# Performance work log

Measured on AMD Instinct MI355X. Metric: run time of the kernel, lower is better.

The kernel has to match this reference:

```python
import jax, jax.numpy as jnp
import numpy as np

B, F, V, E, T, NTOK, G, D = 8192, 64, 1000, 64, 2, 16, 4, 256
LN_EPS = 1e-5


def setup_inputs() -> dict:
    key = jax.random.key(0)
    ks = jax.random.split(key, 5)
    int_feats = jax.random.randint(ks[0], (B, F), 0, V, dtype=jnp.int64)
    missing_mask = jax.random.randint(ks[1], (B, F), 0, 2, dtype=jnp.int32)
    # deterministic seeded permutation of features split into NTOK equal groups
    perm = np.random.default_rng(1234).permutation(F)
    group_idx = jnp.asarray(perm.reshape(NTOK, G), dtype=jnp.int32)
    emb_tables = jax.random.normal(ks[2], (T, F, V, E), jnp.float32) * 0.02
    missing_emb = jax.random.normal(ks[3], (T, F, E), jnp.float32) * 0.02
    kW, kb = jax.random.split(ks[4])
    W = jax.random.normal(kW, (D, E * T), jnp.float32) * (1.0 / np.sqrt(E * T))
    b = jnp.zeros((D,), jnp.float32)
    ln_gamma = jnp.ones((D,), jnp.float32)
    ln_beta = jnp.zeros((D,), jnp.float32)
    return {"int_feats": int_feats, "missing_mask": missing_mask,
            "group_idx": group_idx, "emb_tables": emb_tables,
            "missing_emb": missing_emb, "W": W, "b": b,
            "ln_gamma": ln_gamma, "ln_beta": ln_beta}


def reference(int_feats, missing_mask, group_idx, emb_tables, missing_emb, W, b, ln_gamma, ln_beta):
    f_idx = jnp.arange(F)[None, :]  # (1, F) broadcast with (B, F) ids
    # per-table feature embedding gather: [T, B, F, E]
    feats = jax.vmap(lambda tbl: tbl[f_idx, int_feats])(emb_tables)
    # additive missing embeddings
    mask = missing_mask.astype(feats.dtype)
    feats = feats + mask[None, :, :, None] * missing_emb[:, None, :, :]
    # token-group mean pooling: [T, B, NTOK, G, E] -> [T, B, NTOK, E]
    pooled = feats[:, :, group_idx, :].mean(axis=3)
    # concat tables along feature dim (table order preserved): [B, NTOK, T*E]
    x = jnp.moveaxis(pooled, 0, 2).reshape(B, NTOK, T * E)
    # Linear -> SiLU -> LayerNorm
    h = jax.nn.silu(x @ W.T + b)
    mu = h.mean(-1, keepdims=True)
    var = ((h - mu) ** 2).mean(-1, keepdims=True)
    return (h - mu) * jax.lax.rsqrt(var + LN_EPS) * ln_gamma + ln_beta
```

## Files before the change

### kernel.cpp

```cpp
#include <hip/hip_runtime.h>
#include <math.h>

#define B_    8192
#define F_    64
#define V_    1000
#define E_    64
#define T_    2
#define NTOK_ 16
#define G_    4
#define D_    256
#define K_    128
#define LN_EPS 1e-5f

#define R_    4
#define XSP   136

#define EB_ELEMS (T_*F_*V_*E_)
#define MB_ELEMS (T_*F_*E_)
#define WB_ELEMS (D_*K_)

typedef __attribute__((ext_vector_type(8))) short  frag_ab;
typedef __attribute__((ext_vector_type(4))) float  frag_cd;

template<bool BT> struct GVec;
template<> struct GVec<true>  { using T = uint2;  };
template<> struct GVec<false> { using T = float4; };

static __device__ __forceinline__ unsigned short f2bf(float f) {
    unsigned int u = __float_as_uint(f);
    u += 0x7FFFu + ((u >> 16) & 1u);
    return (unsigned short)(u >> 16);
}
static __device__ __forceinline__ unsigned int pk2(float a, float b) {
    return (unsigned int)f2bf(a) | ((unsigned int)f2bf(b) << 16);
}
static __device__ __forceinline__ void g2f(uint2 v, float& a, float& b, float& c, float& d) {
    a = __uint_as_float(v.x << 16);
    b = __uint_as_float(v.x & 0xFFFF0000u);
    c = __uint_as_float(v.y << 16);
    d = __uint_as_float(v.y & 0xFFFF0000u);
}
static __device__ __forceinline__ void g2f(float4 v, float& a, float& b, float& c, float& d) {
    a = v.x; b = v.y; c = v.z; d = v.w;
}

__global__ __launch_bounds__(256) void convert_w_kernel(const float* __restrict__ W,
                                                        unsigned int* __restrict__ Wb_packed) {
    const int i = blockIdx.x * 256 + threadIdx.x;
    if (i < WB_ELEMS / 2) {
        const float2 v = *(const float2*)(W + (size_t)i * 2);
        Wb_packed[i] = pk2(v.x, v.y);
    }
}

__global__ __launch_bounds__(256) void convert_tbl_kernel(const float* __restrict__ emb,
                                                          const float* __restrict__ miss,
                                                          unsigned int* __restrict__ ebp,
                                                          unsigned int* __restrict__ mbp) {
    const int i = blockIdx.x * 256 + threadIdx.x;
    const int neb = EB_ELEMS / 4;
    if (i < neb) {
        const float4 v = *(const float4*)(emb + (size_t)i * 4);
        ebp[2 * i]     = pk2(v.x, v.y);
        ebp[2 * i + 1] = pk2(v.z, v.w);
    } else if (i < neb + MB_ELEMS / 4) {
        const int j = i - neb;
        const float4 v = *(const float4*)(miss + (size_t)j * 4);
        mbp[2 * j]     = pk2(v.x, v.y);
        mbp[2 * j + 1] = pk2(v.z, v.w);
    }
}

template<bool BT, int MINW>
__global__ __launch_bounds__(256, MINW) void fused_tokenizer_kernel(
    const int*   __restrict__ int_feats,
    const int*   __restrict__ missing_mask,
    const int*   __restrict__ group_idx,
    const float* __restrict__ embf,
    const float* __restrict__ missf,
    const unsigned short* __restrict__ embb,
    const unsigned short* __restrict__ missb,
    const unsigned short* __restrict__ Wb,
    const float* __restrict__ bias,
    const float* __restrict__ gamma,
    const float* __restrict__ beta,
    float*       __restrict__ out)
{
    using VT = typename GVec<BT>::T;

    __shared__ unsigned short xs[2][NTOK_][XSP];
    __shared__ unsigned int   soff[R_][F_];
    __shared__ int            sg[F_];
    __shared__ float          part_s [4][NTOK_];
    __shared__ float          part_ss[4][NTOK_];

    const int tid  = threadIdx.x;
    const int lane = tid & 63;
    const int wave = tid >> 6;
    const int mA   = lane & 15;
    const int q    = lane >> 4;
    const int r0   = blockIdx.x * R_;

    {
        const int rr = tid >> 6, f = tid & 63;
        const int id = int_feats[(r0 + rr) * F_ + f];
        const unsigned int mk = (unsigned int)missing_mask[(r0 + rr) * F_ + f];
        soff[rr][f] = (unsigned int)((f * V_ + id) * E_) | (mk << 31);
        if (tid < F_) sg[tid] = group_idx[tid];
    }

    frag_ab wfr[4][4];
    float bias_r[4], gm_r[4], bt_r[4];
#pragma unroll
    for (int t = 0; t < 4; ++t) {
        const int nrow = wave * 64 + t * 16 + mA;
        const unsigned short* wp = Wb + (size_t)nrow * K_ + 8 * q;
#pragma unroll
        for (int s = 0; s < 4; ++s) wfr[t][s] = *(const frag_ab*)(wp + 32 * s);
        bias_r[t] = bias[nrow];
        gm_r[t]   = gamma[nrow];
        bt_r[t]   = beta[nrow];
    }

    __syncthreads();

    VT  mval[2][G_];
    int fidx[2][G_];
#pragma unroll
    for (int i = 0; i < 2; ++i) {
        const int c = i * 256 + tid, n = c >> 5, r4 = c & 31, tt = r4 >> 4, e = (r4 & 15) * 4;
#pragma unroll
        for (int g = 0; g < G_; ++g) {
            const int f = sg[n * G_ + g];
            fidx[i][g] = f;
            const size_t mo = (size_t)(tt * F_ + f) * E_ + e;
            if constexpr (BT) mval[i][g] = *(const uint2*)(missb + mo);
            else              mval[i][g] = *(const float4*)(missf + mo);
        }
    }

    auto gather_issue = [&](int rr, VT (&gbuf)[2][G_]) {
#pragma unroll
        for (int i = 0; i < 2; ++i) {
            const int c = i * 256 + tid, r4 = c & 31, tt = r4 >> 4, e = (r4 & 15) * 4;
            const size_t tb = (size_t)tt * (F_ * V_ * E_) + e;
#pragma unroll
            for (int g = 0; g < G_; ++g) {
                const unsigned int so = soff[rr][fidx[i][g]] & 0x7FFFFFFFu;
                if constexpr (BT) gbuf[i][g] = *(const uint2*)(embb + tb + so);
                else              gbuf[i][g] = *(const float4*)(embf + tb + so);
            }
        }
    };

    auto pack_write = [&](int rr, unsigned short (&dst)[NTOK_][XSP], VT (&gbuf)[2][G_]) {
#pragma unroll
        for (int i = 0; i < 2; ++i) {
            const int c = i * 256 + tid, n = c >> 5, r4 = c & 31;
            float ax = 0.f, ay = 0.f, az = 0.f, aw = 0.f;
#pragma unroll
            for (int g = 0; g < G_; ++g) {
                float vx, vy, vz, vw, mx, my, mz, mw;
                g2f(gbuf[i][g], vx, vy, vz, vw);
                g2f(mval[i][g], mx, my, mz, mw);
                const float mf = (soff[rr][fidx[i][g]] >> 31) ? 1.f : 0.f;
                ax += vx + mf * mx;
                ay += vy + mf * my;
                az += vz + mf * mz;
                aw += vw + mf * mw;
            }
            *(uint2*)(&dst[n][r4 * 4]) =
                make_uint2(pk2(0.25f * ax, 0.25f * ay), pk2(0.25f * az, 0.25f * aw));
        }
    };

    VT g0[2][G_], g1[2][G_];
    gather_issue(0, g0);

#pragma unroll
    for (int r = 0; r < R_; ++r) {
        if (r + 1 < R_) gather_issue(r + 1, g1);

        pack_write(r, xs[r & 1], g0);
        __syncthreads();

        frag_ab a[4];
#pragma unroll
        for (int s = 0; s < 4; ++s)
            a[s] = *(const frag_ab*)(&xs[r & 1][mA][32 * s + 8 * q]);

        float hv[4][4];
        float ps[4]  = {0.f, 0.f, 0.f, 0.f};
        float pss[4] = {0.f, 0.f, 0.f, 0.f};
#pragma unroll
        for (int t = 0; t < 4; ++t) {
            frag_cd acc = {0.f, 0.f, 0.f, 0.f};
#pragma unroll
            for (int s = 0; s < 4; ++s)
                acc = __builtin_amdgcn_mfma_f32_16x16x32_bf16(a[s], wfr[t][s], acc, 0, 0, 0);
#pragma unroll
            for (int reg = 0; reg < 4; ++reg) {
                const float z = acc[reg] + bias_r[t];
                const float h = z / (1.f + __expf(-z));
                hv[t][reg] = h;
                ps[reg]  += h;
                pss[reg] += h * h;
            }
        }

#pragma unroll
        for (int off = 1; off < 16; off <<= 1) {
#pragma unroll
            for (int reg = 0; reg < 4; ++reg) {
                ps[reg]  += __shfl_xor(ps[reg],  off, 64);
                pss[reg] += __shfl_xor(pss[reg], off, 64);
            }
        }
        if (mA == 0) {
            *(float4*)(&part_s [wave][q * 4]) = make_float4(ps[0],  ps[1],  ps[2],  ps[3]);
            *(float4*)(&part_ss[wave][q * 4]) = make_float4(pss[0], pss[1], pss[2], pss[3]);
        }
        __syncthreads();

        const float4 S0 = *(const float4*)(&part_s [0][q * 4]);
        const float4 S1 = *(const float4*)(&part_s [1][q * 4]);
        const float4 S2 = *(const float4*)(&part_s [2][q * 4]);
        const float4 S3 = *(const float4*)(&part_s [3][q * 4]);
        const float4 T0 = *(const float4*)(&part_ss[0][q * 4]);
        const float4 T1 = *(const float4*)(&part_ss[1][q * 4]);
        const float4 T2 = *(const float4*)(&part_ss[2][q * 4]);
        const float4 T3 = *(const float4*)(&part_ss[3][q * 4]);

        float mu[4], rs[4];
        {
            const float s[4]  = {S0.x + S1.x + S2.x + S3.x, S0.y + S1.y + S2.y + S3.y,
                                 S0.z + S1.z + S2.z + S3.z, S0.w + S1.w + S2.w + S3.w};
            const float ss[4] = {T0.x + T1.x + T2.x + T3.x, T0.y + T1.y + T2.y + T3.y,
                                 T0.z + T1.z + T2.z + T3.z, T0.w + T1.w + T2.w + T3.w};
#pragma unroll
            for (int reg = 0; reg < 4; ++reg) {
                mu[reg] = s[reg] * (1.f / D_);
                const float var = ss[reg] * (1.f / D_) - mu[reg] * mu[reg];
                rs[reg] = rsqrtf(var + LN_EPS);
            }
        }

        const size_t obase = (size_t)(r0 + r) * (NTOK_ * D_);
#pragma unroll
        for (int t = 0; t < 4; ++t) {
            const int col = wave * 64 + t * 16 + mA;
            float* op = out + obase + col;
#pragma unroll
            for (int reg = 0; reg < 4; ++reg)
                op[(size_t)(q * 4 + reg) * D_] =
                    (hv[t][reg] - mu[reg]) * rs[reg] * gm_r[t] + bt_r[t];
        }

#pragma unroll
        for (int i = 0; i < 2; ++i)
#pragma unroll
            for (int g = 0; g < G_; ++g) g0[i][g] = g1[i][g];
    }
}

extern "C" void kernel_launch(void* const* d_in, const int* in_sizes, int n_in,
                              void* d_out, int out_size, void* d_ws, size_t ws_size,
                              hipStream_t stream) {
    const int*   int_feats    = (const int*)  d_in[0];
    const int*   missing_mask = (const int*)  d_in[1];
    const int*   group_idx    = (const int*)  d_in[2];
    const float* emb_tables   = (const float*)d_in[3];
    const float* missing_emb  = (const float*)d_in[4];
    const float* W            = (const float*)d_in[5];
    const float* bias         = (const float*)d_in[6];
    const float* gamma        = (const float*)d_in[7];
    const float* beta         = (const float*)d_in[8];
    float* out = (float*)d_out;

    unsigned short* Wb = (unsigned short*)d_ws;
    convert_w_kernel<<<(WB_ELEMS / 2 + 255) / 256, 256, 0, stream>>>(W, (unsigned int*)Wb);

    const size_t need = 2ull * (WB_ELEMS + MB_ELEMS + EB_ELEMS);
    if (ws_size >= need) {
        unsigned short* Mb = Wb + WB_ELEMS;
        unsigned short* Eb = Mb + MB_ELEMS;
        const int nch = (EB_ELEMS + MB_ELEMS) / 4;
        convert_tbl_kernel<<<(nch + 255) / 256, 256, 0, stream>>>(
            emb_tables, missing_emb, (unsigned int*)Eb, (unsigned int*)Mb);
        fused_tokenizer_kernel<true, 3><<<B_ / R_, 256, 0, stream>>>(
            int_feats, missing_mask, group_idx, nullptr, nullptr, Eb, Mb,
            Wb, bias, gamma, beta, out);
    } else {
        fused_tokenizer_kernel<false, 2><<<B_ / R_, 256, 0, stream>>>(
            int_feats, missing_mask, group_idx, emb_tables, missing_emb, nullptr, nullptr,
            Wb, bias, gamma, beta, out);
    }
}
```

Measured before the change: 262.1 us.

## Process one batch row per block instead of four with software-pipelined gathers

After: 245.1 us. -6.5%, faster.

```diff
diff --git a/kernel.cpp b/kernel.cpp
--- a/kernel.cpp
+++ b/kernel.cpp
@@ -12,7 +12,6 @@
 #define K_    128
 #define LN_EPS 1e-5f
 
-#define R_    4
 #define XSP   136
 
 #define EB_ELEMS (T_*F_*V_*E_)
@@ -55,19 +54,17 @@
 
 __global__ __launch_bounds__(256) void convert_tbl_kernel(const float* __restrict__ emb,
                                                           const float* __restrict__ miss,
-                                                          unsigned int* __restrict__ ebp,
-                                                          unsigned int* __restrict__ mbp) {
+                                                          uint2* __restrict__ ebp,
+                                                          uint2* __restrict__ mbp) {
     const int i = blockIdx.x * 256 + threadIdx.x;
     const int neb = EB_ELEMS / 4;
     if (i < neb) {
         const float4 v = *(const float4*)(emb + (size_t)i * 4);
-        ebp[2 * i]     = pk2(v.x, v.y);
-        ebp[2 * i + 1] = pk2(v.z, v.w);
+        ebp[i] = make_uint2(pk2(v.x, v.y), pk2(v.z, v.w));
     } else if (i < neb + MB_ELEMS / 4) {
         const int j = i - neb;
         const float4 v = *(const float4*)(miss + (size_t)j * 4);
-        mbp[2 * j]     = pk2(v.x, v.y);
-        mbp[2 * j + 1] = pk2(v.z, v.w);
+        mbp[j] = make_uint2(pk2(v.x, v.y), pk2(v.z, v.w));
     }
 }
 
@@ -88,178 +85,148 @@
 {
     using VT = typename GVec<BT>::T;
 
-    __shared__ unsigned short xs[2][NTOK_][XSP];
-    __shared__ unsigned int   soff[R_][F_];
+    __shared__ unsigned short xs[NTOK_][XSP];
+    __shared__ unsigned int   soff[F_];
     __shared__ int            sg[F_];
     __shared__ float          part_s [4][NTOK_];
     __shared__ float          part_ss[4][NTOK_];
 
     const int tid  = threadIdx.x;
+    const int b    = blockIdx.x;
     const int lane = tid & 63;
     const int wave = tid >> 6;
     const int mA   = lane & 15;
     const int q    = lane >> 4;
-    const int r0   = blockIdx.x * R_;
-
-    {
-        const int rr = tid >> 6, f = tid & 63;
-        const int id = int_feats[(r0 + rr) * F_ + f];
-        const unsigned int mk = (unsigned int)missing_mask[(r0 + rr) * F_ + f];
-        soff[rr][f] = (unsigned int)((f * V_ + id) * E_) | (mk << 31);
-        if (tid < F_) sg[tid] = group_idx[tid];
-    }
-
-    frag_ab wfr[4][4];
-    float bias_r[4], gm_r[4], bt_r[4];
+
+    if (tid < F_) {
+        const int id = int_feats[b * F_ + tid];
+        const unsigned int mk = (unsigned int)missing_mask[b * F_ + tid];
+        soff[tid] = (unsigned int)((tid * V_ + id) * E_) | (mk << 31);
+        sg[tid]   = group_idx[tid];
+    }
+    __syncthreads();
+
+    VT    gv[2][G_], mv[2][G_];
+    float msk[2][G_];
+#pragma unroll
+    for (int i = 0; i < 2; ++i) {
+        const int c = i * 256 + tid, n = c >> 5, r4 = c & 31, tt = r4 >> 4, e = (r4 & 15) * 4;
+        const unsigned int tb = (unsigned int)(tt * (F_ * V_ * E_)) + e;
+        const unsigned int mb = (unsigned int)(tt * (F_ * E_)) + e;
+#pragma unroll
+        for (int g = 0; g < G_; ++g) {
+            const int f = sg[n * G_ + g];
+            const unsigned int so = soff[f];
+            msk[i][g] = (so >> 31) ? 1.f : 0.f;
+            const unsigned int eo = tb + (so & 0x7FFFFFFFu);
+            const unsigned int mo = mb + (unsigned int)(f * E_);
+            if constexpr (BT) {
+                gv[i][g] = *(const uint2*)(embb + eo);
+                mv[i][g] = *(const uint2*)(missb + mo);
+            } else {
+                gv[i][g] = *(const float4*)(embf + eo);
+                mv[i][g] = *(const float4*)(missf + mo);
+            }
+        }
+    }
+
+#pragma unroll
+    for (int i = 0; i < 2; ++i) {
+        const int c = i * 256 + tid, n = c >> 5, r4 = c & 31;
+        float ax = 0.f, ay = 0.f, az = 0.f, aw = 0.f;
+#pragma unroll
+        for (int g = 0; g < G_; ++g) {
+            float vx, vy, vz, vw, mx, my, mz, mw;
+            g2f(gv[i][g], vx, vy, vz, vw);
+            g2f(mv[i][g], mx, my, mz, mw);
+            const float m = msk[i][g];
+            ax += vx + m * mx;
+            ay += vy + m * my;
+            az += vz + m * mz;
+            aw += vw + m * mw;
+        }
+        *(uint2*)(&xs[n][r4 * 4]) =
+            make_uint2(pk2(0.25f * ax, 0.25f * ay), pk2(0.25f * az, 0.25f * aw));
+    }
+    __syncthreads();
+
+    frag_ab a[4];
+#pragma unroll
+    for (int s = 0; s < 4; ++s)
+        a[s] = *(const frag_ab*)(&xs[mA][32 * s + 8 * q]);
+
+    float hv[4][4];
+    float ps[4]  = {0.f, 0.f, 0.f, 0.f};
+    float pss[4] = {0.f, 0.f, 0.f, 0.f};
+
 #pragma unroll
     for (int t = 0; t < 4; ++t) {
         const int nrow = wave * 64 + t * 16 + mA;
         const unsigned short* wp = Wb + (size_t)nrow * K_ + 8 * q;
-#pragma unroll
-        for (int s = 0; s < 4; ++s) wfr[t][s] = *(const frag_ab*)(wp + 32 * s);
-        bias_r[t] = bias[nrow];
-        gm_r[t]   = gamma[nrow];
-        bt_r[t]   = beta[nrow];
-    }
-
+        frag_cd acc = {0.f, 0.f, 0.f, 0.f};
+#pragma unroll
+        for (int s = 0; s < 4; ++s) {
+            const frag_ab bfr = *(const frag_ab*)(wp + 32 * s);
+            acc = __builtin_amdgcn_mfma_f32_16x16x32_bf16(a[s], bfr, acc, 0, 0, 0);
+        }
+        const float bn = bias[nrow];
+#pragma unroll
+        for (int reg = 0; reg < 4; ++reg) {
+            const float z = acc[reg] + bn;
+            const float h = z / (1.f + __expf(-z));
+            hv[t][reg] = h;
+            ps[reg]  += h;
+            pss[reg] += h * h;
+        }
+    }
+
+#pragma unroll
+    for (int off = 1; off < 16; off <<= 1) {
+#pragma unroll
+        for (int reg = 0; reg < 4; ++reg) {
+            ps[reg]  += __shfl_xor(ps[reg],  off, 64);
+            pss[reg] += __shfl_xor(pss[reg], off, 64);
+        }
+    }
+    if (mA == 0) {
+        *(float4*)(&part_s [wave][q * 4]) = make_float4(ps[0],  ps[1],  ps[2],  ps[3]);
+        *(float4*)(&part_ss[wave][q * 4]) = make_float4(pss[0], pss[1], pss[2], pss[3]);
+    }
     __syncthreads();
 
-    VT  mval[2][G_];
-    int fidx[2][G_];
-#pragma unroll
-    for (int i = 0; i < 2; ++i) {
-        const int c = i * 256 + tid, n = c >> 5, r4 = c & 31, tt = r4 >> 4, e = (r4 & 15) * 4;
-#pragma unroll
-        for (int g = 0; g < G_; ++g) {
-            const int f = sg[n * G_ + g];
-            fidx[i][g] = f;
-            const size_t mo = (size_t)(tt * F_ + f) * E_ + e;
-            if constexpr (BT) mval[i][g] = *(const uint2*)(missb + mo);
-            else              mval[i][g] = *(const float4*)(missf + mo);
-        }
-    }
-
-    auto gather_issue = [&](int rr, VT (&gbuf)[2][G_]) {
-#pragma unroll
-        for (int i = 0; i < 2; ++i) {
-            const int c = i * 256 + tid, r4 = c & 31, tt = r4 >> 4, e = (r4 & 15) * 4;
-            const size_t tb = (size_t)tt * (F_ * V_ * E_) + e;
-#pragma unroll
-            for (int g = 0; g < G_; ++g) {
-                const unsigned int so = soff[rr][fidx[i][g]] & 0x7FFFFFFFu;
-                if constexpr (BT) gbuf[i][g] = *(const uint2*)(embb + tb + so);
-                else              gbuf[i][g] = *(const float4*)(embf + tb + so);
-            }
-        }
-    };
-
-    auto pack_write = [&](int rr, unsigned short (&dst)[NTOK_][XSP], VT (&gbuf)[2][G_]) {
-#pragma unroll
-        for (int i = 0; i < 2; ++i) {
-            const int c = i * 256 + tid, n = c >> 5, r4 = c & 31;
-            float ax = 0.f, ay = 0.f, az = 0.f, aw = 0.f;
-#pragma unroll
-            for (int g = 0; g < G_; ++g) {
-                float vx, vy, vz, vw, mx, my, mz, mw;
-                g2f(gbuf[i][g], vx, vy, vz, vw);
-                g2f(mval[i][g], mx, my, mz, mw);
-                const float mf = (soff[rr][fidx[i][g]] >> 31) ? 1.f : 0.f;
-                ax += vx + mf * mx;
-                ay += vy + mf * my;
-                az += vz + mf * mz;
-                aw += vw + mf * mw;
-            }
-            *(uint2*)(&dst[n][r4 * 4]) =
-                make_uint2(pk2(0.25f * ax, 0.25f * ay), pk2(0.25f * az, 0.25f * aw));
-        }
-    };
-
-    VT g0[2][G_], g1[2][G_];
-    gather_issue(0, g0);
-
-#pragma unroll
-    for (int r = 0; r < R_; ++r) {
-        if (r + 1 < R_) gather_issue(r + 1, g1);
-
-        pack_write(r, xs[r & 1], g0);
-        __syncthreads();
-
-        frag_ab a[4];
-#pragma unroll
-        for (int s = 0; s < 4; ++s)
-            a[s] = *(const frag_ab*)(&xs[r & 1][mA][32 * s + 8 * q]);
-
-        float hv[4][4];
-        float ps[4]  = {0.f, 0.f, 0.f, 0.f};
-        float pss[4] = {0.f, 0.f, 0.f, 0.f};
-#pragma unroll
-        for (int t = 0; t < 4; ++t) {
-            frag_cd acc = {0.f, 0.f, 0.f, 0.f};
-#pragma unroll
-            for (int s = 0; s < 4; ++s)
-                acc = __builtin_amdgcn_mfma_f32_16x16x32_bf16(a[s], wfr[t][s], acc, 0, 0, 0);
-#pragma unroll
-            for (int reg = 0; reg < 4; ++reg) {
-                const float z = acc[reg] + bias_r[t];
-                const float h = z / (1.f + __expf(-z));
-                hv[t][reg] = h;
-                ps[reg]  += h;
-                pss[reg] += h * h;
-            }
-        }
-
-#pragma unroll
-        for (int off = 1; off < 16; off <<= 1) {
-#pragma unroll
-            for (int reg = 0; reg < 4; ++reg) {
-                ps[reg]  += __shfl_xor(ps[reg],  off, 64);
-                pss[reg] += __shfl_xor(pss[reg], off, 64);
-            }
-        }
-        if (mA == 0) {
-            *(float4*)(&part_s [wave][q * 4]) = make_float4(ps[0],  ps[1],  ps[2],  ps[3]);
-            *(float4*)(&part_ss[wave][q * 4]) = make_float4(pss[0], pss[1], pss[2], pss[3]);
-        }
-        __syncthreads();
-
-        const float4 S0 = *(const float4*)(&part_s [0][q * 4]);
-        const float4 S1 = *(const float4*)(&part_s [1][q * 4]);
-        const float4 S2 = *(const float4*)(&part_s [2][q * 4]);
-        const float4 S3 = *(const float4*)(&part_s [3][q * 4]);
-        const float4 T0 = *(const float4*)(&part_ss[0][q * 4]);
-        const float4 T1 = *(const float4*)(&part_ss[1][q * 4]);
-        const float4 T2 = *(const float4*)(&part_ss[2][q * 4]);
-        const float4 T3 = *(const float4*)(&part_ss[3][q * 4]);
-
-        float mu[4], rs[4];
-        {
-            const float s[4]  = {S0.x + S1.x + S2.x + S3.x, S0.y + S1.y + S2.y + S3.y,
-                                 S0.z + S1.z + S2.z + S3.z, S0.w + S1.w + S2.w + S3.w};
-            const float ss[4] = {T0.x + T1.x + T2.x + T3.x, T0.y + T1.y + T2.y + T3.y,
-                                 T0.z + T1.z + T2.z + T3.z, T0.w + T1.w + T2.w + T3.w};
-#pragma unroll
-            for (int reg = 0; reg < 4; ++reg) {
-                mu[reg] = s[reg] * (1.f / D_);
-                const float var = ss[reg] * (1.f / D_) - mu[reg] * mu[reg];
-                rs[reg] = rsqrtf(var + LN_EPS);
-            }
-        }
-
-        const size_t obase = (size_t)(r0 + r) * (NTOK_ * D_);
-#pragma unroll
-        for (int t = 0; t < 4; ++t) {
-            const int col = wave * 64 + t * 16 + mA;
-            float* op = out + obase + col;
-#pragma unroll
-            for (int reg = 0; reg < 4; ++reg)
-                op[(size_t)(q * 4 + reg) * D_] =
-                    (hv[t][reg] - mu[reg]) * rs[reg] * gm_r[t] + bt_r[t];
-        }
-
-#pragma unroll
-        for (int i = 0; i < 2; ++i)
-#pragma unroll
-            for (int g = 0; g < G_; ++g) g0[i][g] = g1[i][g];
+    const float4 S0 = *(const float4*)(&part_s [0][q * 4]);
+    const float4 S1 = *(const float4*)(&part_s [1][q * 4]);
+    const float4 S2 = *(const float4*)(&part_s [2][q * 4]);
+    const float4 S3 = *(const float4*)(&part_s [3][q * 4]);
+    const float4 T0 = *(const float4*)(&part_ss[0][q * 4]);
+    const float4 T1 = *(const float4*)(&part_ss[1][q * 4]);
+    const float4 T2 = *(const float4*)(&part_ss[2][q * 4]);
+    const float4 T3 = *(const float4*)(&part_ss[3][q * 4]);
+
+    float mu[4], rs[4];
+    {
+        const float s[4]  = {S0.x + S1.x + S2.x + S3.x, S0.y + S1.y + S2.y + S3.y,
+                             S0.z + S1.z + S2.z + S3.z, S0.w + S1.w + S2.w + S3.w};
+        const float ss[4] = {T0.x + T1.x + T2.x + T3.x, T0.y + T1.y + T2.y + T3.y,
+                             T0.z + T1.z + T2.z + T3.z, T0.w + T1.w + T2.w + T3.w};
+#pragma unroll
+        for (int reg = 0; reg < 4; ++reg) {
+            mu[reg] = s[reg] * (1.f / D_);
+            const float var = ss[reg] * (1.f / D_) - mu[reg] * mu[reg];
+            rs[reg] = rsqrtf(var + LN_EPS);
+        }
+    }
+
+    const size_t obase = (size_t)b * (NTOK_ * D_);
+#pragma unroll
+    for (int t = 0; t < 4; ++t) {
+        const int col = wave * 64 + t * 16 + mA;
+        const float gm = gamma[col];
+        const float bb = beta[col];
+        float* op = out + obase + col;
+#pragma unroll
+        for (int reg = 0; reg < 4; ++reg)
+            op[(size_t)(q * 4 + reg) * D_] = (hv[t][reg] - mu[reg]) * rs[reg] * gm + bb;
     }
 }
 
@@ -286,12 +253,12 @@
         unsigned short* Eb = Mb + MB_ELEMS;
         const int nch = (EB_ELEMS + MB_ELEMS) / 4;
         convert_tbl_kernel<<<(nch + 255) / 256, 256, 0, stream>>>(
-            emb_tables, missing_emb, (unsigned int*)Eb, (unsigned int*)Mb);
-        fused_tokenizer_kernel<true, 3><<<B_ / R_, 256, 0, stream>>>(
+            emb_tables, missing_emb, (uint2*)Eb, (uint2*)Mb);
+        fused_tokenizer_kernel<true, 6><<<B_, 256, 0, stream>>>(
             int_feats, missing_mask, group_idx, nullptr, nullptr, Eb, Mb,
             Wb, bias, gamma, beta, out);
     } else {
-        fused_tokenizer_kernel<false, 2><<<B_ / R_, 256, 0, stream>>>(
+        fused_tokenizer_kernel<false, 4><<<B_, 256, 0, stream>>>(
             int_feats, missing_mask, group_idx, emb_tables, missing_emb, nullptr, nullptr,
             Wb, bias, gamma, beta, out);
     }
```
